# Optimization experiments

Measured on AMD Instinct MI355X. Metric: run time of the kernel, lower is better.

Reference implementation:

```python
import jax, jax.numpy as jnp
import numpy as np

B_SZ = 2; L = 512; D_MODEL = 1024
D_STATE = 128; HEADDIM = 64; NGROUPS = 1
D_INNER = 2048; D_SSM = 2048
NHEADS = D_SSM // HEADDIM          # 32
HPG = NHEADS // NGROUPS            # heads per group
HALF = D_STATE // 2
D_IN_PROJ = D_INNER + D_SSM + 2 * NGROUPS * D_STATE + NHEADS + NHEADS + NHEADS * HALF  # 6464
EPS = 1e-5

def _rms(v, w):
    return v * jax.lax.rsqrt(jnp.mean(v * v, axis=-1, keepdims=True) + EPS) * w

def _rope(v, c, s):
    v1, v2 = v[..., :HALF], v[..., HALF:]
    return jnp.concatenate([v1 * c - v2 * s, v2 * c + v1 * s], axis=-1)

def setup_inputs() -> dict:
    key = jax.random.key(0)
    ks = jax.random.split(key, 3)
    rng = np.random.default_rng(0)
    # dt_bias init per module: inverse-softplus of dt ~ LogUniform(dt_min, dt_max)
    dt = np.exp(rng.random(NHEADS) * (np.log(0.1) - np.log(0.001)) + np.log(0.001))
    dt = np.maximum(dt, 1e-4)
    dt_bias = (dt + np.log(-np.expm1(-dt))).astype(np.float32)
    A_log = np.log(rng.uniform(1.0, 16.0, NHEADS)).astype(np.float32)
    return {
        'u': jax.random.normal(ks[0], (B_SZ, L, D_MODEL), jnp.float32),
        'W_in': jax.random.normal(ks[1], (D_MODEL, D_IN_PROJ), jnp.float32) / np.sqrt(D_MODEL),
        'W_out': jax.random.normal(ks[2], (D_INNER, D_MODEL), jnp.float32) / np.sqrt(D_INNER),
        'dt_bias': jnp.asarray(dt_bias),
        'A_log': jnp.asarray(A_log),
        'D': jnp.ones((NHEADS,), jnp.float32),
        'B_bias': jnp.ones((NGROUPS * D_STATE,), jnp.float32),
        'C_bias': jnp.ones((NGROUPS * D_STATE,), jnp.float32),
        'B_norm_w': jnp.ones((D_STATE,), jnp.float32),
        'C_norm_w': jnp.ones((D_STATE,), jnp.float32),
        'norm_w': jnp.ones((D_SSM,), jnp.float32),
    }

def reference(u, W_in, W_out, dt_bias, A_log, D, B_bias, C_bias, B_norm_w, C_norm_w, norm_w):
    b, l, _ = u.shape
    zxbcdt = u @ W_in  # (b, l, d_in_proj)
    s0 = D_INNER; s1 = s0 + D_SSM
    s2 = s1 + NGROUPS * D_STATE; s3 = s2 + NGROUPS * D_STATE
    s4 = s3 + NHEADS; s5 = s4 + NHEADS
    z = zxbcdt[..., :s0]
    x = zxbcdt[..., s0:s1]
    Bv = zxbcdt[..., s1:s2]
    Cv = zxbcdt[..., s2:s3]
    dt_raw = zxbcdt[..., s3:s4]
    lam_raw = zxbcdt[..., s4:s5]
    theta = zxbcdt[..., s5:]
    # BC bias + QK RMSNorm
    Bg = _rms((Bv + B_bias).reshape(b, l, NGROUPS, D_STATE), B_norm_w)
    Cg = _rms((Cv + C_bias).reshape(b, l, NGROUPS, D_STATE), C_norm_w)
    # data-dependent RoPE with cumulative angles, averaged over heads per group
    cum = jnp.cumsum(theta.reshape(b, l, NHEADS, HALF), axis=1)
    cos = jnp.cos(cum).reshape(b, l, NGROUPS, HPG, HALF).mean(3)
    sin = jnp.sin(cum).reshape(b, l, NGROUPS, HPG, HALF).mean(3)
    Bg = _rope(Bg, cos, sin)
    Cg = _rope(Cg, cos, sin)
    # discretization
    dt = jax.nn.softplus(dt_raw + dt_bias)          # (b, l, nheads)
    dA = jnp.exp(dt * (-jnp.exp(A_log)))            # (b, l, nheads)
    x = jax.nn.silu(x).reshape(b, l, NHEADS, HEADDIM)
    # trapezoidal blending of x and B with previous step
    lam = jax.nn.sigmoid(lam_raw)                   # (b, l, nheads)
    x_prev = jnp.pad(x[:, :-1], ((0, 0), (1, 0), (0, 0), (0, 0)))
    x_eff = lam[..., None] * x + (1.0 - lam[..., None]) * x_prev
    B_prev = jnp.pad(Bg[:, :-1], ((0, 0), (1, 0), (0, 0), (0, 0)))
    lam_g = lam.reshape(b, l, NGROUPS, HPG).mean(-1)[..., None]
    B_eff = lam_g * Bg + (1.0 - lam_g) * B_prev
    # selective scan over time
    xs = jnp.moveaxis(x_eff.reshape(b, l, NGROUPS, HPG, HEADDIM), 1, 0)
    dAs = jnp.moveaxis(dA.reshape(b, l, NGROUPS, HPG), 1, 0)
    dts = jnp.moveaxis(dt.reshape(b, l, NGROUPS, HPG), 1, 0)
    Bs = jnp.moveaxis(B_eff, 1, 0)
    Cs = jnp.moveaxis(Cg, 1, 0)
    def step(h, inp):
        dA_t, dt_t, x_t, B_t, C_t = inp
        # h: (b, g, hpg, headdim, d_state)
        h = dA_t[..., None, None] * h + (dt_t[..., None] * x_t)[..., None] * B_t[:, :, None, None, :]
        y_t = jnp.einsum('bgnpd,bgd->bgnp', h, C_t)
        return h, y_t
    h0 = jnp.zeros((b, NGROUPS, HPG, HEADDIM, D_STATE), u.dtype)
    _, ys = jax.lax.scan(step, h0, (dAs, dts, xs, Bs, Cs))
    y = jnp.moveaxis(ys, 0, 1).reshape(b, l, NHEADS, HEADDIM) + D[None, None, :, None] * x_eff
    # gated RMSNorm (norm after gate), then output projection
    y = y.reshape(b, l, D_SSM) * jax.nn.silu(z)
    y = y * jax.lax.rsqrt(jnp.mean(y * y, axis=-1, keepdims=True) + EPS) * norm_w
    return y @ W_out
```

## Files before the change

### kernel.cpp

```cpp
#include <hip/hip_runtime.h>
#include <hip/hip_bf16.h>
#include <cstdint>

#define TOK 1024
#define LSEQ 512
#define DMODEL 1024
#define DPROJ 6464
#define DPROJP 6528
#define DSSM 2048
#define NHEADS 32
#define HEADDIM 64
#define DSTATE 128
#define NCH 8
#define CL 64

typedef __attribute__((ext_vector_type(4))) float f32x4;
typedef _Float16 f16;
typedef __attribute__((ext_vector_type(8))) _Float16 f16x8;
typedef __attribute__((ext_vector_type(4))) _Float16 f16x4;

__device__ __forceinline__ float silu_f(float x){
  return x*__builtin_amdgcn_rcpf(1.f+__expf(-x));
}

__device__ __forceinline__ void gload16(const void* g, void* l){
  __builtin_amdgcn_global_load_lds(
      (const __attribute__((address_space(1))) unsigned int*)g,
      (__attribute__((address_space(3))) unsigned int*)l, 16, 0, 0);
}

__device__ __forceinline__ f16x8 fragH(const float* base){
  f32x4 a = *(const f32x4*)base;
  f32x4 b = *(const f32x4*)(base+4);
  f16x8 h;
  #pragma unroll
  for (int j=0;j<4;j++){ h[j] = (f16)a[j]; h[4+j] = (f16)b[j]; }
  return h;
}

__global__ __launch_bounds__(256) void transqh_kernel(const float* __restrict__ W,
    f16* __restrict__ T, int K, int N)
{
  __shared__ float tile[32][33];
  int tx = threadIdx.x & 31, ty = threadIdx.x >> 5;
  int n = blockIdx.x*32 + tx;
  #pragma unroll
  for (int i=0;i<4;i++){
    int k = blockIdx.y*32 + ty + i*8;
    tile[ty+i*8][tx] = (n < N) ? W[(size_t)k*N + n] : 0.f;
  }
  __syncthreads();
  #pragma unroll
  for (int i=0;i<4;i++){
    int nn = blockIdx.x*32 + ty + i*8;
    int kk = blockIdx.y*32 + tx;
    T[(size_t)nn*K + kk] = (f16)tile[tx][ty+i*8];
  }
}

__global__ __launch_bounds__(256) void cvtH_kernel(const float* __restrict__ A,
    f16* __restrict__ H)
{
  int i = blockIdx.x*256 + threadIdx.x;
  f32x4 v = ((const f32x4*)A)[i];
  f16x4 h;
  #pragma unroll
  for (int j=0;j<4;j++) h[j] = (f16)v[j];
  *(f16x4*)&H[(size_t)i*4] = h;
}

__global__ __launch_bounds__(512) void gemmh_kernel(
    const f16* __restrict__ A, const f16* __restrict__ B,
    float* __restrict__ C, int K, int kLen, int ldc, int nbn, int chunk)
{
  __shared__ ushort sA[2][8192], sB[2][8192];
  int bid = blockIdx.x;
  int newL = (bid & 7)*chunk + (bid >> 3);
  int bm = newL & 7;
  int pan = newL >> 3;
  int bn = pan % nbn;
  int z  = pan / nbn;
  int k0 = z * kLen;
  C += (size_t)z * 1024 * ldc;

  int tid = threadIdx.x;
  int wid = tid >> 6, lane = tid & 63;
  int wr = wid >> 2, wc = wid & 3;
  int fr = lane & 15, kq = lane >> 4;
  f32x4 acc[4][2] = {};

  int srow = tid & 127;
  int skg  = (tid >> 7) & 3;
  const f16* gA = A + (size_t)(bm*128+srow)*K + k0 + skg*8;
  const f16* gB = B + (size_t)(bn*128+srow)*K + k0 + skg*8;

  int rA = kq*1024 + (wr*64 + fr)*8;
  int rB = kq*1024 + (wc*32 + fr)*8;
  int NK = kLen >> 6;

#define STAGE(buf, kk) { \
    const f16* pa = gA + (kk)*64; \
    const f16* pb = gB + (kk)*64; \
    gload16(pa,      &sA[buf][tid*8]); \
    gload16(pa + 32, &sA[buf][tid*8 + 4096]); \
    gload16(pb,      &sB[buf][tid*8]); \
    gload16(pb + 32, &sB[buf][tid*8 + 4096]); \
  }

  STAGE(0, 0)
  STAGE(1, 1)

  for (int ks=0; ks<NK; ks++){
    int cur = ks & 1;
    if (ks == NK-1) asm volatile("s_waitcnt vmcnt(0)" ::: "memory");
    else            asm volatile("s_waitcnt vmcnt(4)" ::: "memory");
    __builtin_amdgcn_s_barrier();
    f16x8 af0[4], af1[4], bf0[2], bf1[2];
    #pragma unroll
    for (int i=0;i<4;i++){
      af0[i] = *(const f16x8*)&sA[cur][rA + i*128];
      af1[i] = *(const f16x8*)&sA[cur][rA + 4096 + i*128];
    }
    #pragma unroll
    for (int j=0;j<2;j++){
      bf0[j] = *(const f16x8*)&sB[cur][rB + j*128];
      bf1[j] = *(const f16x8*)&sB[cur][rB + 4096 + j*128];
    }
    asm volatile("s_waitcnt lgkmcnt(0)" ::: "memory");
    __builtin_amdgcn_sched_barrier(0);
    __builtin_amdgcn_s_barrier();
    if (ks+2 < NK) STAGE(cur, ks+2)
    #pragma unroll
    for (int i=0;i<4;i++)
      #pragma unroll
      for (int j=0;j<2;j++)
        acc[i][j] = __builtin_amdgcn_mfma_f32_16x16x32_f16(af0[i], bf0[j], acc[i][j], 0,0,0);
    #pragma unroll
    for (int i=0;i<4;i++)
      #pragma unroll
      for (int j=0;j<2;j++)
        acc[i][j] = __builtin_amdgcn_mfma_f32_16x16x32_f16(af1[i], bf1[j], acc[i][j], 0,0,0);
  }
#undef STAGE
  int rq = kq * 4;
  #pragma unroll
  for (int i=0;i<4;i++){
    #pragma unroll
    for (int j=0;j<2;j++){
      int row = bm*128 + wr*64 + i*16 + rq;
      int col = bn*128 + wc*32 + j*16 + fr;
      #pragma unroll
      for (int q=0;q<4;q++)
        C[(size_t)(row+q)*ldc + col] = acc[i][j][q];
    }
  }
}

__global__ __launch_bounds__(256) void red4_kernel(const float* __restrict__ P, float* __restrict__ O){
  int i = blockIdx.x*256 + threadIdx.x;
  f32x4 v = ((const f32x4*)P)[i];
  v += ((const f32x4*)P)[i + 262144];
  v += ((const f32x4*)P)[i + 2*262144];
  v += ((const f32x4*)P)[i + 3*262144];
  ((f32x4*)O)[i] = v;
}

__global__ __launch_bounds__(256) void thT_kernel(const float* __restrict__ zx,
    float* __restrict__ thT)
{
  __shared__ float tile[64][65];
  int ci = blockIdx.x, li = blockIdx.y, bb = blockIdx.z;
  int tx = threadIdx.x & 63, ty = threadIdx.x >> 6;
  const float* src = zx + (size_t)(bb*LSEQ + li*64)*DPROJP + 4416 + ci*64;
  #pragma unroll
  for (int i=0;i<16;i++){
    int r = ty + i*4;
    tile[r][tx] = src[(size_t)r*DPROJP + tx];
  }
  __syncthreads();
  float* dst = thT + ((size_t)bb*2048 + ci*64)*512 + (size_t)li*64;
  #pragma unroll
  for (int i=0;i<16;i++){
    int r = ty + i*4;
    dst[(size_t)r*512 + tx] = tile[tx][r];
  }
}

__global__ __launch_bounds__(512) void cum2_kernel(const float* __restrict__ thT,
    float* __restrict__ cosm, float* __restrict__ sinm)
{
  __shared__ float wsum[8];
  int blk = blockIdx.x;
  int half = blk & 1, hd = (blk >> 1) & 63, b = blk >> 7;
  int l = threadIdx.x, lane = l & 63, w = l >> 6;
  float accc = 0.f, accs = 0.f;
  const float* base = thT + (size_t)b*2048*512 + (size_t)(half*16)*64*512 + (size_t)hd*512;
  for (int h = 0; h < 16; h++){
    float x = base[(size_t)h*64*512 + l];
    #pragma unroll
    for (int m=1; m<64; m<<=1){
      float v = __shfl_up(x, m, 64);
      if (lane >= m) x += v;
    }
    if (lane == 63) wsum[w] = x;
    __syncthreads();
    float pre = 0.f;
    for (int i=0;i<w;i++) pre += wsum[i];
    x += pre;
    float s, c;
    __sincosf(x, &s, &c);
    accc += c; accs += s;
    __syncthreads();
  }
  int t = b*LSEQ + l;
  cosm[half*TOK*64 + t*64+hd] = accc*(1.f/32.f);
  sinm[half*TOK*64 + t*64+hd] = accs*(1.f/32.f);
}

__global__ __launch_bounds__(256) void ew_kernel(const float* __restrict__ zx,
    const float* __restrict__ cosm, const float* __restrict__ sinm,
    const float* __restrict__ dt_bias, const float* __restrict__ A_log,
    const float* __restrict__ B_bias, const float* __restrict__ C_bias,
    const float* __restrict__ Bnw, const float* __restrict__ Cnw,
    float* __restrict__ Bg, float* __restrict__ Cg, float4* __restrict__ scal)
{
  int t = blockIdx.x; int tid = threadIdx.x;
  __shared__ float red[256];
  __shared__ float nb[128], nc[128];
  const float* row = zx + (size_t)t*DPROJP;
  float v;
  if (tid < 128) v = row[4096 + tid] + B_bias[tid];
  else           v = row[4224 + (tid-128)] + C_bias[tid-128];
  red[tid] = v*v;
  __syncthreads();
  #pragma unroll
  for (int s=64; s>0; s>>=1){
    if ((tid & 127) < s) red[tid] += red[tid + s];
    __syncthreads();
  }
  float ms = red[(tid < 128) ? 0 : 128] * (1.f/128.f);
  float rs = rsqrtf(ms + 1e-5f);
  float w  = (tid < 128) ? Bnw[tid] : Cnw[tid-128];
  float nv = v * rs * w;
  if (tid < 128) nb[tid] = nv; else nc[tid-128] = nv;
  __syncthreads();
  if (tid < 64){
    float c = cosm[t*64+tid] + cosm[TOK*64 + t*64+tid];
    float s = sinm[t*64+tid] + sinm[TOK*64 + t*64+tid];
    float a = nb[tid], bq = nb[tid+64];
    Bg[(size_t)t*128 + tid]      = a*c - bq*s;
    Bg[(size_t)t*128 + 64 + tid] = bq*c + a*s;
  } else if (tid < 128){
    int i = tid - 64;
    float c = cosm[t*64+i] + cosm[TOK*64 + t*64+i];
    float s = sinm[t*64+i] + sinm[TOK*64 + t*64+i];
    float a = nc[i], bq = nc[i+64];
    Cg[(size_t)t*128 + i]      = a*c - bq*s;
    Cg[(size_t)t*128 + 64 + i] = bq*c + a*s;
  } else if (tid < 160){
    int hh = tid - 128;
    float dtr = row[4352 + hh] + dt_bias[hh];
    float dtv = (dtr > 20.f) ? dtr : log1pf(expf(dtr));
    float dA  = expf(-dtv * expf(A_log[hh]));
    float lr  = row[4384 + hh];
    float lam = 1.f/(1.f + expf(-lr));
    float lg = lam;
    #pragma unroll
    for (int m=1;m<32;m<<=1) lg += __shfl_xor(lg, m, 64);
    lg *= (1.f/32.f);
    scal[(size_t)t*32 + hh] = make_float4(dtv, dA, lam, lg);
  }
}

__global__ __launch_bounds__(256, 1) void scanA_kernel(
    const float* __restrict__ zx, const float* __restrict__ Bg,
    const float* __restrict__ Cg, const float4* __restrict__ scal,
    const float* __restrict__ A_log, const float* __restrict__ Dp,
    float* __restrict__ ypart, float* __restrict__ hcarry,
    float* __restrict__ clog, float* __restrict__ AtotB)
{
  __shared__ __align__(16) float smC[64*132];
  __shared__ __align__(16) float smB[64*132];
  __shared__ __align__(16) float smBT[128*68];
  __shared__ __align__(16) float smX[64*68];
  __shared__ __align__(16) float sDt[64], sLam[64], sLg[64], sCl[64], sW[64];
  float* sSp = smC;

  int blk = blockIdx.x;
  int c = blk & 7, h = (blk>>3)&31, b = blk>>8;
  int idx = blk;
  int t0 = b*LSEQ + c*CL;
  int tid = threadIdx.x;
  int w = tid >> 6, lane = tid & 63;
  int fr = lane & 15, kq = lane >> 4;

  {
    int s = tid >> 2, dq4 = (tid & 3) * 32;
    const float* src = Cg + (size_t)(t0+s)*128 + dq4;
    float* dst = smC + s*132 + dq4;
    #pragma unroll
    for (int i=0;i<8;i++) *(f32x4*)(dst + i*4) = *(const f32x4*)(src + i*4);
  }
  if (tid < 64){
    float4 sc = scal[(size_t)(t0+tid)*32 + h];
    float a  = __expf(A_log[h]);
    float cl = -sc.x * a * 1.44269504088896f;
    #pragma unroll
    for (int m=1; m<64; m<<=1){
      float v = __shfl_up(cl, m, 64);
      if (lane >= m) cl += v;
    }
    float cl63 = __shfl(cl, 63, 64);
    sDt[tid] = sc.x; sLam[tid] = sc.z; sLg[tid] = sc.w;
    sCl[tid] = cl;
    sW[tid]  = exp2f(cl63 - cl) * sc.x;
    clog[(size_t)idx*64 + tid] = cl;
    if (tid == 63) AtotB[idx] = exp2f(cl63);
  }
  __syncthreads();

  {
    int s = tid >> 2, dq4 = (tid & 3) * 32;
    float lg = sLg[s], wgt = sW[s];
    bool zp = (s == 0 && c == 0);
    const float* bc_p = Bg + (size_t)(t0+s)*128 + dq4;
    const float* bp_p = Bg + (size_t)(t0+s-1)*128 + dq4;
    #pragma unroll
    for (int i=0;i<32;i+=4){
      f32x4 bc = *(const f32x4*)(bc_p + i);
      f32x4 bp = zp ? (f32x4){0,0,0,0} : *(const f32x4*)(bp_p + i);
      f32x4 be = bp + lg*(bc - bp);
      *(f32x4*)(smB + s*132 + dq4 + i) = be;
      smBT[(dq4+i+0)*68 + s] = be.x * wgt;
      smBT[(dq4+i+1)*68 + s] = be.y * wgt;
      smBT[(dq4+i+2)*68 + s] = be.z * wgt;
      smBT[(dq4+i+3)*68 + s] = be.w * wgt;
    }
  }
  {
    int p = tid & 63, sg = tid >> 6;
    int s0 = sg*16;
    const float* xbase = zx + 2048 + h*64 + p;
    float xp_ = 0.f;
    if (!(s0 == 0 && c == 0))
      xp_ = silu_f(xbase[(size_t)(t0+s0-1)*DPROJP]);
    #pragma unroll
    for (int i=0;i<16;i++){
      int s = s0 + i;
      float xs = silu_f(xbase[(size_t)(t0+s)*DPROJP]);
      smX[p*68 + s] = xp_ + sLam[s]*(xs - xp_);
      xp_ = xs;
    }
  }
  __syncthreads();

  int tq = w >> 1, sq = w & 1;
  f32x4 acc1[2][2] = {};
  #pragma unroll
  for (int kt=0; kt<4; kt++){
    f16x8 ah[2], bh[2];
    #pragma unroll
    for (int i=0;i<2;i++)
      ah[i] = fragH(smC + (tq*32 + i*16 + fr)*132 + kt*32 + kq*8);
    #pragma unroll
    for (int j=0;j<2;j++)
      bh[j] = fragH(smB + (sq*32 + j*16 + fr)*132 + kt*32 + kq*8);
    #pragma unroll
    for (int i=0;i<2;i++)
      #pragma unroll
      for (int j=0;j<2;j++)
        acc1[i][j] = __builtin_amdgcn_mfma_f32_16x16x32_f16(ah[i], bh[j], acc1[i][j], 0,0,0);
  }
  #pragma unroll
  for (int i=0;i<2;i++){
    int tb = tq*32 + i*16 + kq*4;
    f32x4 clt = *(const f32x4*)&sCl[tb];
    #pragma unroll
    for (int j=0;j<2;j++){
      int scol = sq*32 + j*16 + fr;
      float cls = sCl[scol], dts = sDt[scol];
      #pragma unroll
      for (int q=0;q<4;q++){
        float m = (tb+q >= scol) ? exp2f(clt[q]-cls)*dts : 0.f;
        acc1[i][j][q] *= m;
      }
    }
  }
  __syncthreads();
  #pragma unroll
  for (int i=0;i<2;i++){
    int tb = tq*32 + i*16 + kq*4;
    #pragma unroll
    for (int j=0;j<2;j++){
      int scol = sq*32 + j*16 + fr;
      #pragma unroll
      for (int q=0;q<4;q++)
        sSp[(tb+q)*68 + scol] = acc1[i][j][q];
    }
  }
  __syncthreads();

  float Dh = Dp[h];
  {
    f32x4 acc2[2][2] = {};
    #pragma unroll
    for (int kt=0; kt<2; kt++){
      f16x8 ah[2], bh[2];
      #pragma unroll
      for (int i=0;i<2;i++)
        ah[i] = fragH(sSp + (tq*32 + i*16 + fr)*68 + kt*32 + kq*8);
      #pragma unroll
      for (int j=0;j<2;j++)
        bh[j] = fragH(smX + (sq*32 + j*16 + fr)*68 + kt*32 + kq*8);
      #pragma unroll
      for (int i=0;i<2;i++)
        #pragma unroll
        for (int j=0;j<2;j++)
          acc2[i][j] = __builtin_amdgcn_mfma_f32_16x16x32_f16(ah[i], bh[j], acc2[i][j], 0,0,0);
    }
    #pragma unroll
    for (int i=0;i<2;i++){
      int tb = tq*32 + i*16 + kq*4;
      #pragma unroll
      for (int j=0;j<2;j++){
        int pc = sq*32 + j*16 + fr;
        #pragma unroll
        for (int q=0;q<4;q++){
          float y = acc2[i][j][q] + Dh * smX[pc*68 + tb + q];
          ypart[(size_t)(t0+tb+q)*DSSM + h*64 + pc] = y;
        }
      }
    }
  }

  {
    f32x4 acc4[2][4] = {};
    int ph = w >> 1, dh = w & 1;
    #pragma unroll
    for (int kt=0; kt<2; kt++){
      f16x8 ah[2], bh[4];
      #pragma unroll
      for (int i=0;i<2;i++)
        ah[i] = fragH(smX + (ph*32 + i*16 + fr)*68 + kt*32 + kq*8);
      #pragma unroll
      for (int j=0;j<4;j++)
        bh[j] = fragH(smBT + (dh*64 + j*16 + fr)*68 + kt*32 + kq*8);
      #pragma unroll
      for (int i=0;i<2;i++)
        #pragma unroll
        for (int j=0;j<4;j++)
          acc4[i][j] = __builtin_amdgcn_mfma_f32_16x16x32_f16(ah[i], bh[j], acc4[i][j], 0,0,0);
    }
    size_t hb = (size_t)idx * 64 * 128;
    #pragma unroll
    for (int i=0;i<2;i++){
      int pb = ph*32 + i*16 + kq*4;
      #pragma unroll
      for (int j=0;j<4;j++){
        int dc = dh*64 + j*16 + fr;
        #pragma unroll
        for (int q=0;q<4;q++)
          hcarry[hb + (size_t)(pb+q)*128 + dc] = acc4[i][j][q];
      }
    }
  }
}

__global__ __launch_bounds__(256) void scan2_kernel(float* __restrict__ hcarry,
    const float* __restrict__ AtotB)
{
  int idx = blockIdx.x*256 + threadIdx.x;
  int d = idx & 127, pp = (idx >> 7) & 63, h = (idx >> 13) & 31, b = idx >> 18;
  size_t base = ((size_t)(b*32+h)*512 + pp)*128 + d;
  float Hin = 0.f;
  #pragma unroll
  for (int c=0; c<NCH; c++){
    float Atot = AtotB[(b*32+h)*8 + c];
    float S = hcarry[base + (size_t)c*8192];
    hcarry[base + (size_t)c*8192] = Hin;
    Hin = Atot*Hin + S;
  }
}

__global__ __launch_bounds__(256) void scanB_kernel(
    const float* __restrict__ Cg, const float* __restrict__ hcarry,
    const float* __restrict__ clog, float* __restrict__ ypart)
{
  __shared__ __align__(16) float smC[64*132];
  __shared__ __align__(16) float smH[64*132];
  __shared__ __align__(16) float sK[64];
  int blk = blockIdx.x;
  int c = blk & 7, h = (blk>>3)&31, b = blk>>8;
  int idx = blk;
  int t0 = b*LSEQ + c*CL;
  int tid = threadIdx.x;
  int w = tid >> 6, lane = tid & 63;
  int fr = lane & 15, kq = lane >> 4;
  {
    int s = tid >> 2, dq4 = (tid & 3) * 32;
    const float* src = Cg + (size_t)(t0+s)*128 + dq4;
    float* dst = smC + s*132 + dq4;
    #pragma unroll
    for (int i=0;i<8;i++) *(f32x4*)(dst + i*4) = *(const f32x4*)(src + i*4);
    const float* hs = hcarry + (size_t)idx*8192 + (size_t)s*128 + dq4;
    float* hd = smH + s*132 + dq4;
    #pragma unroll
    for (int i=0;i<8;i++) *(f32x4*)(hd + i*4) = *(const f32x4*)(hs + i*4);
  }
  if (tid < 64) sK[tid] = exp2f(clog[(size_t)idx*64 + tid]);
  __syncthreads();

  int tq = w >> 1, pq = w & 1;
  f32x4 acc[2][2] = {};
  #pragma unroll
  for (int kt=0; kt<4; kt++){
    f16x8 ah[2], bh[2];
    #pragma unroll
    for (int i=0;i<2;i++)
      ah[i] = fragH(smC + (tq*32 + i*16 + fr)*132 + kt*32 + kq*8);
    #pragma unroll
    for (int j=0;j<2;j++)
      bh[j] = fragH(smH + (pq*32 + j*16 + fr)*132 + kt*32 + kq*8);
    #pragma unroll
    for (int i=0;i<2;i++)
      #pragma unroll
      for (int j=0;j<2;j++)
        acc[i][j] = __builtin_amdgcn_mfma_f32_16x16x32_f16(ah[i], bh[j], acc[i][j], 0,0,0);
  }
  #pragma unroll
  for (int i=0;i<2;i++){
    int tb = tq*32 + i*16 + kq*4;
    f32x4 kv = *(const f32x4*)&sK[tb];
    #pragma unroll
    for (int j=0;j<2;j++){
      int pc = pq*32 + j*16 + fr;
      #pragma unroll
      for (int q=0;q<4;q++)
        ypart[(size_t)TOK*DSSM + (size_t)(t0+tb+q)*DSSM + h*64 + pc] = acc[i][j][q]*kv[q];
    }
  }
}

__global__ __launch_bounds__(256) void fin_kernel(const float* __restrict__ zx,
    const float* __restrict__ ypart, const float* __restrict__ normw,
    f16* __restrict__ yf)
{
  int t = blockIdx.x; int tid = threadIdx.x;
  __shared__ float red[256];
  float vloc[8];
  float ss = 0.f;
  #pragma unroll
  for (int i=0;i<8;i++){
    int cc = tid + i*256;
    float y = ypart[(size_t)t*DSSM + cc]
            + ypart[(size_t)(TOK + t)*DSSM + cc];
    float z = zx[(size_t)t*DPROJP + cc];
    float v = y * (z / (1.f + expf(-z)));
    vloc[i] = v; ss += v*v;
  }
  red[tid] = ss; __syncthreads();
  #pragma unroll
  for (int s=128; s>0; s>>=1){ if (tid < s) red[tid] += red[tid+s]; __syncthreads(); }
  float rs = rsqrtf(red[0]*(1.f/2048.f) + 1e-5f);
  #pragma unroll
  for (int i=0;i<8;i++){
    int cc = tid + i*256;
    yf[(size_t)t*DSSM + cc] = (f16)(vloc[i]*rs*normw[cc]);
  }
}

extern "C" void kernel_launch(void* const* d_in, const int* in_sizes, int n_in,
                              void* d_out, int out_size, void* d_ws, size_t ws_size,
                              hipStream_t stream)
{
  const float* u      = (const float*)d_in[0];
  const float* W_in   = (const float*)d_in[1];
  const float* W_out  = (const float*)d_in[2];
  const float* dt_bias= (const float*)d_in[3];
  const float* A_log  = (const float*)d_in[4];
  const float* Dp     = (const float*)d_in[5];
  const float* B_bias = (const float*)d_in[6];
  const float* C_bias = (const float*)d_in[7];
  const float* Bnw    = (const float*)d_in[8];
  const float* Cnw    = (const float*)d_in[9];
  const float* normw  = (const float*)d_in[10];
  float* out = (float*)d_out;

  char* ws = (char*)d_ws;
  size_t o = 0;
  auto alloc = [&](size_t bytes)->char*{
    char* r = ws + o; o = (o + bytes + 255) & ~(size_t)255; return r;
  };
  f16*  WT   = (f16*)alloc((size_t)DPROJP*DMODEL*2);
  f16*  WoT  = (f16*)alloc((size_t)DMODEL*DSSM*2);
  f16*  uhf  = (f16*)alloc((size_t)TOK*DMODEL*2);
  f16*  yf   = (f16*)alloc((size_t)TOK*DSSM*2);
  float*  zx   = (float*)alloc((size_t)TOK*DPROJP*4);
  float*  thT  = (float*)alloc((size_t)2*2048*512*4);
  float*  cosm = (float*)alloc((size_t)2*TOK*64*4);
  float*  sinm = (float*)alloc((size_t)2*TOK*64*4);
  float*  Bgb  = (float*)alloc((size_t)TOK*128*4);
  float*  Cgb  = (float*)alloc((size_t)TOK*128*4);
  float4* scal = (float4*)alloc((size_t)TOK*32*16);
  float*  ypart= (float*)alloc((size_t)2*TOK*DSSM*4);
  float*  hcarry=(float*)alloc((size_t)2*32*NCH*64*128*4);
  float*  clog = (float*)alloc((size_t)512*64*4);
  float*  AtotB= (float*)alloc((size_t)512*4);
  float*  Cpart =(float*)alloc((size_t)4*TOK*DMODEL*4);

  transqh_kernel<<<dim3(DPROJP/32, DMODEL/32), dim3(256), 0, stream>>>(W_in, WT, DMODEL, DPROJ);
  transqh_kernel<<<dim3(DMODEL/32, DSSM/32),   dim3(256), 0, stream>>>(W_out, WoT, DSSM, DMODEL);
  cvtH_kernel<<<dim3(TOK*DMODEL/1024), dim3(256), 0, stream>>>(u, uhf);

  gemmh_kernel<<<dim3(408), dim3(512), 0, stream>>>(uhf, WT, zx, DMODEL, DMODEL, DPROJP, 51, 51);

  thT_kernel<<<dim3(32, 8, 2), dim3(256), 0, stream>>>(zx, thT);
  cum2_kernel<<<dim3(256), dim3(512), 0, stream>>>(thT, cosm, sinm);

  ew_kernel<<<dim3(TOK), dim3(256), 0, stream>>>(zx, cosm, sinm, dt_bias, A_log,
                                                 B_bias, C_bias, Bnw, Cnw, Bgb, Cgb, scal);

  scanA_kernel<<<dim3(512),  dim3(256), 0, stream>>>(zx, Bgb, Cgb, scal, A_log, Dp,
                                                     ypart, hcarry, clog, AtotB);
  scan2_kernel<<<dim3(2048), dim3(256), 0, stream>>>(hcarry, AtotB);
  scanB_kernel<<<dim3(512),  dim3(256), 0, stream>>>(Cgb, hcarry, clog, ypart);

  fin_kernel<<<dim3(TOK), dim3(256), 0, stream>>>(zx, ypart, normw, yf);

  gemmh_kernel<<<dim3(256), dim3(512), 0, stream>>>(yf, WoT, Cpart, DSSM, 512, DMODEL, 8, 32);
  red4_kernel<<<dim3(TOK*DMODEL/1024), dim3(256), 0, stream>>>(Cpart, out);
}
```

Measured before the change: 140.5 us.

## Store B/C and scan shared tiles in fp16, fuse prep kernels

Changes the B and C intermediates and all scan shared-memory tiles from fp32 to fp16, so MFMA fragments load directly with no per-fragment conversion. Shared memory per block roughly halves, which allows two blocks per CU via launch bounds. Also merges the two weight transposes and the input conversion into one prep kernel to save launches. Rounding intermediates such as the scores, B_eff and the carried state to fp16 adds precision error.

Measured after the change: 129.3 us. 1.09x faster.

```diff
diff --git a/kernel.cpp b/kernel.cpp
--- a/kernel.cpp
+++ b/kernel.cpp
@@ -18,6 +18,7 @@
 typedef _Float16 f16;
 typedef __attribute__((ext_vector_type(8))) _Float16 f16x8;
 typedef __attribute__((ext_vector_type(4))) _Float16 f16x4;
+typedef __attribute__((ext_vector_type(8))) ushort u16x8;
 
 __device__ __forceinline__ float silu_f(float x){
   return x*__builtin_amdgcn_rcpf(1.f+__expf(-x));
@@ -29,44 +30,39 @@
       (__attribute__((address_space(3))) unsigned int*)l, 16, 0, 0);
 }
 
-__device__ __forceinline__ f16x8 fragH(const float* base){
-  f32x4 a = *(const f32x4*)base;
-  f32x4 b = *(const f32x4*)(base+4);
-  f16x8 h;
-  #pragma unroll
-  for (int j=0;j<4;j++){ h[j] = (f16)a[j]; h[4+j] = (f16)b[j]; }
-  return h;
-}
-
-__global__ __launch_bounds__(256) void transqh_kernel(const float* __restrict__ W,
-    f16* __restrict__ T, int K, int N)
-{
-  __shared__ float tile[32][33];
-  int tx = threadIdx.x & 31, ty = threadIdx.x >> 5;
-  int n = blockIdx.x*32 + tx;
-  #pragma unroll
-  for (int i=0;i<4;i++){
-    int k = blockIdx.y*32 + ty + i*8;
-    tile[ty+i*8][tx] = (n < N) ? W[(size_t)k*N + n] : 0.f;
-  }
-  __syncthreads();
-  #pragma unroll
-  for (int i=0;i<4;i++){
-    int nn = blockIdx.x*32 + ty + i*8;
-    int kk = blockIdx.y*32 + tx;
-    T[(size_t)nn*K + kk] = (f16)tile[tx][ty+i*8];
-  }
-}
-
-__global__ __launch_bounds__(256) void cvtH_kernel(const float* __restrict__ A,
-    f16* __restrict__ H)
-{
-  int i = blockIdx.x*256 + threadIdx.x;
-  f32x4 v = ((const f32x4*)A)[i];
-  f16x4 h;
-  #pragma unroll
-  for (int j=0;j<4;j++) h[j] = (f16)v[j];
-  *(f16x4*)&H[(size_t)i*4] = h;
+__global__ __launch_bounds__(256) void prep_kernel(
+    const float* __restrict__ W_in, const float* __restrict__ W_out,
+    const float* __restrict__ u,
+    f16* __restrict__ WT, f16* __restrict__ WoT, f16* __restrict__ uhf)
+{
+  int b = blockIdx.x;
+  if (b < 6528 + 2048){
+    __shared__ float tile[32][33];
+    const float* W; f16* T; int K, N, bx, by;
+    if (b < 6528){ W = W_in;  T = WT;  K = DMODEL; N = DPROJ;  bx = b % 204;      by = b / 204; }
+    else         { int ib = b - 6528; W = W_out; T = WoT; K = DSSM; N = DMODEL; bx = ib & 31; by = ib >> 5; }
+    int tx = threadIdx.x & 31, ty = threadIdx.x >> 5;
+    int n = bx*32 + tx;
+    #pragma unroll
+    for (int i=0;i<4;i++){
+      int k = by*32 + ty + i*8;
+      tile[ty+i*8][tx] = (n < N) ? W[(size_t)k*N + n] : 0.f;
+    }
+    __syncthreads();
+    #pragma unroll
+    for (int i=0;i<4;i++){
+      int nn = bx*32 + ty + i*8;
+      int kk = by*32 + tx;
+      T[(size_t)nn*K + kk] = (f16)tile[tx][ty+i*8];
+    }
+  } else {
+    int i = (b - 8576)*256 + threadIdx.x;
+    f32x4 v = ((const f32x4*)u)[i];
+    f16x4 h;
+    #pragma unroll
+    for (int j=0;j<4;j++) h[j] = (f16)v[j];
+    *(f16x4*)&uhf[(size_t)i*4] = h;
+  }
 }
 
 __global__ __launch_bounds__(512) void gemmh_kernel(
@@ -222,7 +218,7 @@
     const float* __restrict__ dt_bias, const float* __restrict__ A_log,
     const float* __restrict__ B_bias, const float* __restrict__ C_bias,
     const float* __restrict__ Bnw, const float* __restrict__ Cnw,
-    float* __restrict__ Bg, float* __restrict__ Cg, float4* __restrict__ scal)
+    f16* __restrict__ Bg, f16* __restrict__ Cg, float4* __restrict__ scal)
 {
   int t = blockIdx.x; int tid = threadIdx.x;
   __shared__ float red[256];
@@ -248,15 +244,15 @@
     float c = cosm[t*64+tid] + cosm[TOK*64 + t*64+tid];
     float s = sinm[t*64+tid] + sinm[TOK*64 + t*64+tid];
     float a = nb[tid], bq = nb[tid+64];
-    Bg[(size_t)t*128 + tid]      = a*c - bq*s;
-    Bg[(size_t)t*128 + 64 + tid] = bq*c + a*s;
+    Bg[(size_t)t*128 + tid]      = (f16)(a*c - bq*s);
+    Bg[(size_t)t*128 + 64 + tid] = (f16)(bq*c + a*s);
   } else if (tid < 128){
     int i = tid - 64;
     float c = cosm[t*64+i] + cosm[TOK*64 + t*64+i];
     float s = sinm[t*64+i] + sinm[TOK*64 + t*64+i];
     float a = nc[i], bq = nc[i+64];
-    Cg[(size_t)t*128 + i]      = a*c - bq*s;
-    Cg[(size_t)t*128 + 64 + i] = bq*c + a*s;
+    Cg[(size_t)t*128 + i]      = (f16)(a*c - bq*s);
+    Cg[(size_t)t*128 + 64 + i] = (f16)(bq*c + a*s);
   } else if (tid < 160){
     int hh = tid - 128;
     float dtr = row[4352 + hh] + dt_bias[hh];
@@ -272,19 +268,21 @@
   }
 }
 
-__global__ __launch_bounds__(256, 1) void scanA_kernel(
-    const float* __restrict__ zx, const float* __restrict__ Bg,
-    const float* __restrict__ Cg, const float4* __restrict__ scal,
+#define CST 136
+#define SST 72
+__global__ __launch_bounds__(256, 2) void scanA_kernel(
+    const float* __restrict__ zx, const f16* __restrict__ Bg,
+    const f16* __restrict__ Cg, const float4* __restrict__ scal,
     const float* __restrict__ A_log, const float* __restrict__ Dp,
     float* __restrict__ ypart, float* __restrict__ hcarry,
     float* __restrict__ clog, float* __restrict__ AtotB)
 {
-  __shared__ __align__(16) float smC[64*132];
-  __shared__ __align__(16) float smB[64*132];
-  __shared__ __align__(16) float smBT[128*68];
-  __shared__ __align__(16) float smX[64*68];
+  __shared__ __align__(16) f16 smC[64*CST];
+  __shared__ __align__(16) f16 smB[64*CST];
+  __shared__ __align__(16) f16 smBT[128*SST];
+  __shared__ __align__(16) f16 smX[64*SST];
   __shared__ __align__(16) float sDt[64], sLam[64], sLg[64], sCl[64], sW[64];
-  float* sSp = smC;
+  f16* sSp = smC;
 
   int blk = blockIdx.x;
   int c = blk & 7, h = (blk>>3)&31, b = blk>>8;
@@ -296,10 +294,10 @@
 
   {
     int s = tid >> 2, dq4 = (tid & 3) * 32;
-    const float* src = Cg + (size_t)(t0+s)*128 + dq4;
-    float* dst = smC + s*132 + dq4;
-    #pragma unroll
-    for (int i=0;i<8;i++) *(f32x4*)(dst + i*4) = *(const f32x4*)(src + i*4);
+    const ushort* src = (const ushort*)(Cg + (size_t)(t0+s)*128 + dq4);
+    ushort* dst = (ushort*)(smC + s*CST + dq4);
+    #pragma unroll
+    for (int i=0;i<4;i++) *(u16x8*)(dst + i*8) = *(const u16x8*)(src + i*8);
   }
   if (tid < 64){
     float4 sc = scal[(size_t)(t0+tid)*32 + h];
@@ -323,18 +321,22 @@
     int s = tid >> 2, dq4 = (tid & 3) * 32;
     float lg = sLg[s], wgt = sW[s];
     bool zp = (s == 0 && c == 0);
-    const float* bc_p = Bg + (size_t)(t0+s)*128 + dq4;
-    const float* bp_p = Bg + (size_t)(t0+s-1)*128 + dq4;
+    const f16* bc_p = Bg + (size_t)(t0+s)*128 + dq4;
+    const f16* bp_p = Bg + (size_t)(t0+s-1)*128 + dq4;
     #pragma unroll
     for (int i=0;i<32;i+=4){
-      f32x4 bc = *(const f32x4*)(bc_p + i);
-      f32x4 bp = zp ? (f32x4){0,0,0,0} : *(const f32x4*)(bp_p + i);
-      f32x4 be = bp + lg*(bc - bp);
-      *(f32x4*)(smB + s*132 + dq4 + i) = be;
-      smBT[(dq4+i+0)*68 + s] = be.x * wgt;
-      smBT[(dq4+i+1)*68 + s] = be.y * wgt;
-      smBT[(dq4+i+2)*68 + s] = be.z * wgt;
-      smBT[(dq4+i+3)*68 + s] = be.w * wgt;
+      f16x4 bc4 = *(const f16x4*)(bc_p + i);
+      f16x4 bp4 = {0,0,0,0};
+      if (!zp) bp4 = *(const f16x4*)(bp_p + i);
+      f16x4 be4;
+      #pragma unroll
+      for (int e=0;e<4;e++){
+        float bc = (float)bc4[e], bp = (float)bp4[e];
+        float be = bp + lg*(bc - bp);
+        be4[e] = (f16)be;
+        smBT[(dq4+i+e)*SST + s] = (f16)(be * wgt);
+      }
+      *(f16x4*)(smB + s*CST + dq4 + i) = be4;
     }
   }
   {
@@ -348,7 +350,7 @@
     for (int i=0;i<16;i++){
       int s = s0 + i;
       float xs = silu_f(xbase[(size_t)(t0+s)*DPROJP]);
-      smX[p*68 + s] = xp_ + sLam[s]*(xs - xp_);
+      smX[p*SST + s] = (f16)(xp_ + sLam[s]*(xs - xp_));
       xp_ = xs;
     }
   }
@@ -361,10 +363,10 @@
     f16x8 ah[2], bh[2];
     #pragma unroll
     for (int i=0;i<2;i++)
-      ah[i] = fragH(smC + (tq*32 + i*16 + fr)*132 + kt*32 + kq*8);
+      ah[i] = *(const f16x8*)&smC[(tq*32 + i*16 + fr)*CST + kt*32 + kq*8];
     #pragma unroll
     for (int j=0;j<2;j++)
-      bh[j] = fragH(smB + (sq*32 + j*16 + fr)*132 + kt*32 + kq*8);
+      bh[j] = *(const f16x8*)&smB[(sq*32 + j*16 + fr)*CST + kt*32 + kq*8];
     #pragma unroll
     for (int i=0;i<2;i++)
       #pragma unroll
@@ -395,7 +397,7 @@
       int scol = sq*32 + j*16 + fr;
       #pragma unroll
       for (int q=0;q<4;q++)
-        sSp[(tb+q)*68 + scol] = acc1[i][j][q];
+        sSp[(tb+q)*SST + scol] = (f16)acc1[i][j][q];
     }
   }
   __syncthreads();
@@ -408,10 +410,10 @@
       f16x8 ah[2], bh[2];
       #pragma unroll
       for (int i=0;i<2;i++)
-        ah[i] = fragH(sSp + (tq*32 + i*16 + fr)*68 + kt*32 + kq*8);
+        ah[i] = *(const f16x8*)&sSp[(tq*32 + i*16 + fr)*SST + kt*32 + kq*8];
       #pragma unroll
       for (int j=0;j<2;j++)
-        bh[j] = fragH(smX + (sq*32 + j*16 + fr)*68 + kt*32 + kq*8);
+        bh[j] = *(const f16x8*)&smX[(sq*32 + j*16 + fr)*SST + kt*32 + kq*8];
       #pragma unroll
       for (int i=0;i<2;i++)
         #pragma unroll
@@ -426,7 +428,7 @@
         int pc = sq*32 + j*16 + fr;
         #pragma unroll
         for (int q=0;q<4;q++){
-          float y = acc2[i][j][q] + Dh * smX[pc*68 + tb + q];
+          float y = acc2[i][j][q] + Dh * (float)smX[pc*SST + tb + q];
           ypart[(size_t)(t0+tb+q)*DSSM + h*64 + pc] = y;
         }
       }
@@ -441,10 +443,10 @@
       f16x8 ah[2], bh[4];
       #pragma unroll
       for (int i=0;i<2;i++)
-        ah[i] = fragH(smX + (ph*32 + i*16 + fr)*68 + kt*32 + kq*8);
+        ah[i] = *(const f16x8*)&smX[(ph*32 + i*16 + fr)*SST + kt*32 + kq*8];
       #pragma unroll
       for (int j=0;j<4;j++)
-        bh[j] = fragH(smBT + (dh*64 + j*16 + fr)*68 + kt*32 + kq*8);
+        bh[j] = *(const f16x8*)&smBT[(dh*64 + j*16 + fr)*SST + kt*32 + kq*8];
       #pragma unroll
       for (int i=0;i<2;i++)
         #pragma unroll
@@ -483,11 +485,11 @@
 }
 
 __global__ __launch_bounds__(256) void scanB_kernel(
-    const float* __restrict__ Cg, const float* __restrict__ hcarry,
+    const f16* __restrict__ Cg, const float* __restrict__ hcarry,
     const float* __restrict__ clog, float* __restrict__ ypart)
 {
-  __shared__ __align__(16) float smC[64*132];
-  __shared__ __align__(16) float smH[64*132];
+  __shared__ __align__(16) f16 smC[64*CST];
+  __shared__ __align__(16) f16 smH[64*CST];
   __shared__ __align__(16) float sK[64];
   int blk = blockIdx.x;
   int c = blk & 7, h = (blk>>3)&31, b = blk>>8;
@@ -498,14 +500,19 @@
   int fr = lane & 15, kq = lane >> 4;
   {
     int s = tid >> 2, dq4 = (tid & 3) * 32;
-    const float* src = Cg + (size_t)(t0+s)*128 + dq4;
-    float* dst = smC + s*132 + dq4;
-    #pragma unroll
-    for (int i=0;i<8;i++) *(f32x4*)(dst + i*4) = *(const f32x4*)(src + i*4);
+    const ushort* src = (const ushort*)(Cg + (size_t)(t0+s)*128 + dq4);
+    ushort* dst = (ushort*)(smC + s*CST + dq4);
+    #pragma unroll
+    for (int i=0;i<4;i++) *(u16x8*)(dst + i*8) = *(const u16x8*)(src + i*8);
     const float* hs = hcarry + (size_t)idx*8192 + (size_t)s*128 + dq4;
-    float* hd = smH + s*132 + dq4;
-    #pragma unroll
-    for (int i=0;i<8;i++) *(f32x4*)(hd + i*4) = *(const f32x4*)(hs + i*4);
+    #pragma unroll
+    for (int i=0;i<32;i+=4){
+      f32x4 v = *(const f32x4*)(hs + i);
+      f16x4 hv;
+      #pragma unroll
+      for (int e=0;e<4;e++) hv[e] = (f16)v[e];
+      *(f16x4*)(smH + s*CST + dq4 + i) = hv;
+    }
   }
   if (tid < 64) sK[tid] = exp2f(clog[(size_t)idx*64 + tid]);
   __syncthreads();
@@ -517,10 +524,10 @@
     f16x8 ah[2], bh[2];
     #pragma unroll
     for (int i=0;i<2;i++)
-      ah[i] = fragH(smC + (tq*32 + i*16 + fr)*132 + kt*32 + kq*8);
+      ah[i] = *(const f16x8*)&smC[(tq*32 + i*16 + fr)*CST + kt*32 + kq*8];
     #pragma unroll
     for (int j=0;j<2;j++)
-      bh[j] = fragH(smH + (pq*32 + j*16 + fr)*132 + kt*32 + kq*8);
+      bh[j] = *(const f16x8*)&smH[(pq*32 + j*16 + fr)*CST + kt*32 + kq*8];
     #pragma unroll
     for (int i=0;i<2;i++)
       #pragma unroll
@@ -599,8 +606,8 @@
   float*  thT  = (float*)alloc((size_t)2*2048*512*4);
   float*  cosm = (float*)alloc((size_t)2*TOK*64*4);
   float*  sinm = (float*)alloc((size_t)2*TOK*64*4);
-  float*  Bgb  = (float*)alloc((size_t)TOK*128*4);
-  float*  Cgb  = (float*)alloc((size_t)TOK*128*4);
+  f16*   Bgb  = (f16*)alloc((size_t)TOK*128*2);
+  f16*   Cgb  = (f16*)alloc((size_t)TOK*128*2);
   float4* scal = (float4*)alloc((size_t)TOK*32*16);
   float*  ypart= (float*)alloc((size_t)2*TOK*DSSM*4);
   float*  hcarry=(float*)alloc((size_t)2*32*NCH*64*128*4);
@@ -608,9 +615,7 @@
   float*  AtotB= (float*)alloc((size_t)512*4);
   float*  Cpart =(float*)alloc((size_t)4*TOK*DMODEL*4);
 
-  transqh_kernel<<<dim3(DPROJP/32, DMODEL/32), dim3(256), 0, stream>>>(W_in, WT, DMODEL, DPROJ);
-  transqh_kernel<<<dim3(DMODEL/32, DSSM/32),   dim3(256), 0, stream>>>(W_out, WoT, DSSM, DMODEL);
-  cvtH_kernel<<<dim3(TOK*DMODEL/1024), dim3(256), 0, stream>>>(u, uhf);
+  prep_kernel<<<dim3(9600), dim3(256), 0, stream>>>(W_in, W_out, u, WT, WoT, uhf);
 
   gemmh_kernel<<<dim3(408), dim3(512), 0, stream>>>(uhf, WT, zx, DMODEL, DMODEL, DPROJP, 51, 51);
 
```
